# Kernel tuning notes

Hardware: AMD Instinct MI355X
Metric: run time of the kernel (lower is better)

The kernel has to match this reference:

```python
import jax, jax.numpy as jnp
import numpy as np
import math

FACIL_RATE = 2.0
FIRE_THRESH = 0.85
MAX_GATE = 8.0
N_BUF = 512
TOP_K_FRAC = 0.1
B, T, D = 4, 4096, 2048


def _gelu(x):
    c = math.sqrt(2.0 / math.pi)
    return 0.5 * x * (1.0 + jnp.tanh(c * (x + 0.044715 * x * x * x)))


def setup_inputs() -> dict:
    key = jax.random.key(0)
    k1, k2, k3 = jax.random.split(key, 3)
    x = jax.random.normal(k1, (B, T, D), dtype=jnp.float32)
    log_strength = jnp.asarray(0.0, dtype=jnp.float32)
    # Steady-state ring buffer: keys = normalized mean vectors, masks = top-k(|mean|) indicators
    means = jax.random.normal(k2, (N_BUF, D), dtype=jnp.float32)
    buf_keys = means / jnp.linalg.norm(means, axis=-1, keepdims=True)
    top_k = max(1, int(D * TOP_K_FRAC))  # 204
    _, top_idx = jax.lax.top_k(jnp.abs(means), top_k)  # (N_BUF, top_k)
    buf_masks = jnp.zeros((N_BUF, D), dtype=jnp.float32).at[
        jnp.arange(N_BUF)[:, None], top_idx].set(1.0)
    facil = 1.0 + 3.0 * jax.random.uniform(k3, (N_BUF,), dtype=jnp.float32)
    valid_mask = jnp.ones((N_BUF,), dtype=bool)
    return {"x": x, "log_strength": log_strength, "buf_keys": buf_keys,
            "buf_masks": buf_masks, "facil": facil, "valid_mask": valid_mask}


def reference(x, log_strength, buf_keys, buf_masks, facil, valid_mask):
    # Steady-state (pass1_complete) path of GELU277.forward
    y = _gelu(x)  # (B, T, D)
    # m_curr = y.detach().flatten(0,1).mean(0)  -> stop_gradient as in torch no_grad
    m_curr = jax.lax.stop_gradient(y).reshape(-1, y.shape[-1]).mean(0)  # (D,)
    q = m_curr / jnp.linalg.norm(m_curr)
    sims = buf_keys @ q                      # (N_BUF,) cosine similarities
    sims = jnp.where(valid_mask, sims, -1.0)
    nearest = jnp.argmax(sims)
    sim_max = sims[nearest]
    # facil[nearest] *= FACIL_RATE if fired, then read (.item() in torch -> constant)
    f = jax.lax.stop_gradient(facil[nearest]) * jnp.where(sim_max > FIRE_THRESH, FACIL_RATE, 1.0)
    # strength.item() in torch -> no grad through log_strength
    strength = jax.lax.stop_gradient(jnp.clip(jnp.exp(log_strength), 0.01, 5.0))
    k_amp = jnp.minimum(1.0 + strength * (f - 1.0), MAX_GATE)
    topk_mask = jax.lax.stop_gradient(buf_masks[nearest])  # (D,)
    gate = 1.0 + (k_amp - 1.0) * topk_mask
    return y * gate[None, None, :]
```

## Files before the change

### kernel.cpp

```cpp
#include <hip/hip_runtime.h>
#include <math.h>

#define DCOLS 2048
#define NROWS 16384
#define NBUF  512
#define NBP   1024

typedef float v4f __attribute__((ext_vector_type(4)));

__device__ __forceinline__ float gelu_f(float x) {
    const float c = 0.7978845608028654f;
    float u = c * (x + 0.044715f * x * x * x);
    float e = __expf(2.0f * u);
    float t = 1.0f - 2.0f * __builtin_amdgcn_rcpf(1.0f + e);
    return 0.5f * x * (1.0f + t);
}

__global__ __launch_bounds__(512) void k_part(const float* __restrict__ x,
                                              float* __restrict__ part,
                                              int* __restrict__ cnt) {
    int t = threadIdx.x;
    int col = t * 4;
    if (blockIdx.x == 0 && t == 0) *cnt = 0;
    float a0 = 0.f, a1 = 0.f, a2 = 0.f, a3 = 0.f;
#pragma unroll 4
    for (int r = blockIdx.x; r < NROWS; r += NBP) {
        float4 v = *reinterpret_cast<const float4*>(x + (size_t)r * DCOLS + col);
        a0 += gelu_f(v.x); a1 += gelu_f(v.y); a2 += gelu_f(v.z); a3 += gelu_f(v.w);
    }
    float4 st; st.x = a0; st.y = a1; st.z = a2; st.w = a3;
    *reinterpret_cast<float4*>(part + (size_t)blockIdx.x * DCOLS + col) = st;
}

__global__ __launch_bounds__(256) void k_reduce(const float* __restrict__ part,
                                                float* __restrict__ colsum) {
    __shared__ float4 lds[64][4];
    int t  = threadIdx.x;
    int tx = t & 3;
    int ty = t >> 2;
    int c  = blockIdx.x * 16 + tx * 4;
    float4 acc = {0.f, 0.f, 0.f, 0.f};
    for (int i = ty; i < NBP; i += 64) {
        float4 p = *reinterpret_cast<const float4*>(part + (size_t)i * DCOLS + c);
        acc.x += p.x; acc.y += p.y; acc.z += p.z; acc.w += p.w;
    }
    lds[ty][tx] = acc;
    __syncthreads();
    for (int off = 32; off; off >>= 1) {
        if (ty < off) {
            float4 o = lds[ty + off][tx];
            float4 m = lds[ty][tx];
            m.x += o.x; m.y += o.y; m.z += o.z; m.w += o.w;
            lds[ty][tx] = m;
        }
        __syncthreads();
    }
    if (ty == 0)
        *reinterpret_cast<float4*>(colsum + c) = lds[0][tx];
}

__global__ __launch_bounds__(256) void k_sims_gate(const float* __restrict__ keys,
                                                   const float* __restrict__ colsum,
                                                   float* __restrict__ s,
                                                   const float* __restrict__ log_strength,
                                                   const float* __restrict__ facil,
                                                   const float* __restrict__ masks,
                                                   float* __restrict__ gate,
                                                   int* __restrict__ counter) {
    __shared__ float red[256];
    __shared__ int   redi[256];
    __shared__ bool  last;
    int row = blockIdx.x;
    int t = threadIdx.x;
    const float* kr = keys + (size_t)row * DCOLS;
    int j = t * 8;
    float4 k0 = *reinterpret_cast<const float4*>(kr + j);
    float4 k1 = *reinterpret_cast<const float4*>(kr + j + 4);
    float4 c0 = *reinterpret_cast<const float4*>(colsum + j);
    float4 c1 = *reinterpret_cast<const float4*>(colsum + j + 4);
    float acc = k0.x*c0.x + k0.y*c0.y + k0.z*c0.z + k0.w*c0.w
              + k1.x*c1.x + k1.y*c1.y + k1.z*c1.z + k1.w*c1.w;
    for (int off = 32; off; off >>= 1) acc += __shfl_down(acc, off);
    if ((t & 63) == 0) red[t >> 6] = acc;
    __syncthreads();
    if (t == 0) {
        s[row] = red[0] + red[1] + red[2] + red[3];
        __threadfence();
        last = (atomicAdd(counter, 1) == (int)gridDim.x - 1);
    }
    __syncthreads();
    if (!last) return;
    __threadfence();

    float n2 = 0.f;
    for (int k = t; k < DCOLS; k += 256) { float v = colsum[k]; n2 += v * v; }
    red[t] = n2; __syncthreads();
    for (int off = 128; off; off >>= 1) {
        if (t < off) red[t] += red[t + off];
        __syncthreads();
    }
    float norm = sqrtf(red[0]);
    __syncthreads();

    float best = -1e30f; int bi = 0x7fffffff;
    for (int k = t; k < NBUF; k += 256) {
        float v = s[k];
        if (v > best || (v == best && k < bi)) { best = v; bi = k; }
    }
    red[t] = best; redi[t] = bi; __syncthreads();
    for (int off = 128; off; off >>= 1) {
        if (t < off) {
            float ov = red[t + off]; int oi = redi[t + off];
            if (ov > red[t] || (ov == red[t] && oi < redi[t])) { red[t] = ov; redi[t] = oi; }
        }
        __syncthreads();
    }
    int nearest = redi[0];
    float sim_max = red[0] / norm;

    float strength = __expf(log_strength[0]);
    strength = fminf(fmaxf(strength, 0.01f), 5.0f);
    float f = facil[nearest] * (sim_max > 0.85f ? 2.0f : 1.0f);
    float k_amp = fminf(1.0f + strength * (f - 1.0f), 8.0f);

    const float* mrow = masks + (size_t)nearest * DCOLS;
    for (int k = t; k < DCOLS; k += 256)
        gate[k] = 1.0f + (k_amp - 1.0f) * mrow[k];
}

__global__ __launch_bounds__(256) void k_scale(const float* __restrict__ x,
                                               const float* __restrict__ gate,
                                               float* __restrict__ out) {
    int t = threadIdx.x;
    int col = t * 8;
    float4 g0 = *reinterpret_cast<const float4*>(gate + col);
    float4 g1 = *reinterpret_cast<const float4*>(gate + col + 4);
    for (int r = blockIdx.x; r < NROWS; r += gridDim.x) {
        size_t off = (size_t)r * DCOLS + col;
        float4 v0 = *reinterpret_cast<const float4*>(x + off);
        float4 v1 = *reinterpret_cast<const float4*>(x + off + 4);
        v4f o0, o1;
        o0.x = gelu_f(v0.x) * g0.x; o0.y = gelu_f(v0.y) * g0.y;
        o0.z = gelu_f(v0.z) * g0.z; o0.w = gelu_f(v0.w) * g0.w;
        o1.x = gelu_f(v1.x) * g1.x; o1.y = gelu_f(v1.y) * g1.y;
        o1.z = gelu_f(v1.z) * g1.z; o1.w = gelu_f(v1.w) * g1.w;
        *reinterpret_cast<v4f*>(out + off)     = o0;
        *reinterpret_cast<v4f*>(out + off + 4) = o1;
    }
}

__global__ __launch_bounds__(512) void k_colsum_atomic(const float* __restrict__ x,
                                                       float* __restrict__ colsum) {
    int t = threadIdx.x;
    int col = t * 4;
    float a0 = 0.f, a1 = 0.f, a2 = 0.f, a3 = 0.f;
    for (int r = blockIdx.x; r < NROWS; r += gridDim.x) {
        float4 v = *reinterpret_cast<const float4*>(x + (size_t)r * DCOLS + col);
        a0 += gelu_f(v.x); a1 += gelu_f(v.y); a2 += gelu_f(v.z); a3 += gelu_f(v.w);
    }
    atomicAdd(&colsum[col + 0], a0);
    atomicAdd(&colsum[col + 1], a1);
    atomicAdd(&colsum[col + 2], a2);
    atomicAdd(&colsum[col + 3], a3);
}

extern "C" void kernel_launch(void* const* d_in, const int* in_sizes, int n_in,
                              void* d_out, int out_size, void* d_ws, size_t ws_size,
                              hipStream_t stream) {
    const float* x            = (const float*)d_in[0];
    const float* log_strength = (const float*)d_in[1];
    const float* keys         = (const float*)d_in[2];
    const float* masks        = (const float*)d_in[3];
    const float* facil        = (const float*)d_in[4];
    float* out = (float*)d_out;
    float* ws  = (float*)d_ws;

    float* colsum = ws;
    float* s      = ws + 2048;
    float* gate   = ws + 2560;
    int*   cnt    = (int*)(ws + 4608);
    float* part   = ws + 4864;

    size_t need = (size_t)(4864 + (size_t)NBP * DCOLS) * sizeof(float);

    if (ws_size >= need) {
        k_part<<<NBP, 512, 0, stream>>>(x, part, cnt);
        k_reduce<<<DCOLS / 16, 256, 0, stream>>>(part, colsum);
    } else {
        (void)hipMemsetAsync(ws, 0, 4864 * sizeof(float), stream);
        k_colsum_atomic<<<512, 512, 0, stream>>>(x, colsum);
    }
    k_sims_gate<<<NBUF, 256, 0, stream>>>(keys, colsum, s, log_strength,
                                          facil, masks, gate, cnt);
    k_scale<<<2048, 256, 0, stream>>>(x, gate, out);
}
```

Baseline: 94.70 us.

## Write GELU output in the reduction pass and rescale only gated columns

The first pass now stores the GELU result to the output while it accumulates column sums, using nontemporal loads of x. The final kernel no longer recomputes GELU from x. It reads the stored output back and multiplies only the 4-column groups whose gate is not 1, skipping whole threads whose gates are all 1. The atomic fallback for a small workspace is removed. The aim is to avoid recomputing GELU and to skip untouched columns, at the cost of a full extra write in pass one plus read-modify-write traffic on scattered gated columns, which at cache-line granularity may touch most lines anyway.

After: 116.4 us. +22.9%, slower.

```diff
diff --git a/kernel.cpp b/kernel.cpp
--- a/kernel.cpp
+++ b/kernel.cpp
@@ -17,6 +17,7 @@
 }
 
 __global__ __launch_bounds__(512) void k_part(const float* __restrict__ x,
+                                              float* __restrict__ out,
                                               float* __restrict__ part,
                                               int* __restrict__ cnt) {
     int t = threadIdx.x;
@@ -25,8 +26,12 @@
     float a0 = 0.f, a1 = 0.f, a2 = 0.f, a3 = 0.f;
 #pragma unroll 4
     for (int r = blockIdx.x; r < NROWS; r += NBP) {
-        float4 v = *reinterpret_cast<const float4*>(x + (size_t)r * DCOLS + col);
-        a0 += gelu_f(v.x); a1 += gelu_f(v.y); a2 += gelu_f(v.z); a3 += gelu_f(v.w);
+        size_t off = (size_t)r * DCOLS + col;
+        v4f v = __builtin_nontemporal_load(reinterpret_cast<const v4f*>(x + off));
+        v4f y;
+        y.x = gelu_f(v.x); y.y = gelu_f(v.y); y.z = gelu_f(v.z); y.w = gelu_f(v.w);
+        a0 += y.x; a1 += y.y; a2 += y.z; a3 += y.w;
+        *reinterpret_cast<v4f*>(out + off) = y;
     }
     float4 st; st.x = a0; st.y = a1; st.z = a2; st.w = a3;
     *reinterpret_cast<float4*>(part + (size_t)blockIdx.x * DCOLS + col) = st;
@@ -128,40 +133,28 @@
         gate[k] = 1.0f + (k_amp - 1.0f) * mrow[k];
 }
 
-__global__ __launch_bounds__(256) void k_scale(const float* __restrict__ x,
-                                               const float* __restrict__ gate,
-                                               float* __restrict__ out) {
+__global__ __launch_bounds__(256) void k_rescale(float* __restrict__ out,
+                                                 const float* __restrict__ gate) {
     int t = threadIdx.x;
     int col = t * 8;
     float4 g0 = *reinterpret_cast<const float4*>(gate + col);
     float4 g1 = *reinterpret_cast<const float4*>(gate + col + 4);
+    bool a0 = (g0.x != 1.f) | (g0.y != 1.f) | (g0.z != 1.f) | (g0.w != 1.f);
+    bool a1 = (g1.x != 1.f) | (g1.y != 1.f) | (g1.z != 1.f) | (g1.w != 1.f);
+    if (!a0 && !a1) return;
     for (int r = blockIdx.x; r < NROWS; r += gridDim.x) {
         size_t off = (size_t)r * DCOLS + col;
-        float4 v0 = *reinterpret_cast<const float4*>(x + off);
-        float4 v1 = *reinterpret_cast<const float4*>(x + off + 4);
-        v4f o0, o1;
-        o0.x = gelu_f(v0.x) * g0.x; o0.y = gelu_f(v0.y) * g0.y;
-        o0.z = gelu_f(v0.z) * g0.z; o0.w = gelu_f(v0.w) * g0.w;
-        o1.x = gelu_f(v1.x) * g1.x; o1.y = gelu_f(v1.y) * g1.y;
-        o1.z = gelu_f(v1.z) * g1.z; o1.w = gelu_f(v1.w) * g1.w;
-        *reinterpret_cast<v4f*>(out + off)     = o0;
-        *reinterpret_cast<v4f*>(out + off + 4) = o1;
+        if (a0) {
+            float4 v = *reinterpret_cast<const float4*>(out + off);
+            v.x *= g0.x; v.y *= g0.y; v.z *= g0.z; v.w *= g0.w;
+            *reinterpret_cast<float4*>(out + off) = v;
+        }
+        if (a1) {
+            float4 v = *reinterpret_cast<const float4*>(out + off + 4);
+            v.x *= g1.x; v.y *= g1.y; v.z *= g1.z; v.w *= g1.w;
+            *reinterpret_cast<float4*>(out + off + 4) = v;
+        }
     }
-}
-
-__global__ __launch_bounds__(512) void k_colsum_atomic(const float* __restrict__ x,
-                                                       float* __restrict__ colsum) {
-    int t = threadIdx.x;
-    int col = t * 4;
-    float a0 = 0.f, a1 = 0.f, a2 = 0.f, a3 = 0.f;
-    for (int r = blockIdx.x; r < NROWS; r += gridDim.x) {
-        float4 v = *reinterpret_cast<const float4*>(x + (size_t)r * DCOLS + col);
-        a0 += gelu_f(v.x); a1 += gelu_f(v.y); a2 += gelu_f(v.z); a3 += gelu_f(v.w);
-    }
-    atomicAdd(&colsum[col + 0], a0);
-    atomicAdd(&colsum[col + 1], a1);
-    atomicAdd(&colsum[col + 2], a2);
-    atomicAdd(&colsum[col + 3], a3);
 }
 
 extern "C" void kernel_launch(void* const* d_in, const int* in_sizes, int n_in,
@@ -181,16 +174,9 @@
     int*   cnt    = (int*)(ws + 4608);
     float* part   = ws + 4864;
 
-    size_t need = (size_t)(4864 + (size_t)NBP * DCOLS) * sizeof(float);
-
-    if (ws_size >= need) {
-        k_part<<<NBP, 512, 0, stream>>>(x, part, cnt);
-        k_reduce<<<DCOLS / 16, 256, 0, stream>>>(part, colsum);
-    } else {
-        (void)hipMemsetAsync(ws, 0, 4864 * sizeof(float), stream);
-        k_colsum_atomic<<<512, 512, 0, stream>>>(x, colsum);
-    }
+    k_part<<<NBP, 512, 0, stream>>>(x, out, part, cnt);
+    k_reduce<<<DCOLS / 16, 256, 0, stream>>>(part, colsum);
     k_sims_gate<<<NBUF, 256, 0, stream>>>(keys, colsum, s, log_strength,
                                           facil, masks, gate, cnt);
-    k_scale<<<2048, 256, 0, stream>>>(x, gate, out);
+    k_rescale<<<2048, 256, 0, stream>>>(out, gate);
 }
```
